# Performance work log

Hardware: AMD Instinct MI355X
Metric: run time of the kernel (lower is better)

Reference implementation:

```python
import jax, jax.numpy as jnp
import numpy as np

ALPHA = 0.2  # LeakyReLU negative slope


def _gat_layer(x, W, a):
    """One GraphAttentionLayer (concat=True -> elu output).
    x: (B,N,Din); W: (Din,F); a: (2F,1).
    Faithful to source: adj mask is computed then discarded (softmax over raw e),
    so adj does not enter the math. Uses the additive decomposition
    e_ij = leakyrelu(a1.h_i + a2.h_j) which is mathematically identical to the
    dense (N,N,2F) concat in the original.
    """
    h = x @ W                      # (B,N,F)
    F = W.shape[1]
    a1, a2 = a[:F, 0], a[F:, 0]    # (F,), (F,)
    f1 = h @ a1                    # (B,N)
    f2 = h @ a2                    # (B,N)
    e = jax.nn.leaky_relu(f1[:, :, None] + f2[:, None, :], negative_slope=ALPHA)  # (B,N,N)
    att = jax.nn.softmax(e, axis=-1)
    h_prime = jnp.einsum('bnm,bmf->bnf', att, h)
    return jax.nn.elu(h_prime)


def setup_inputs() -> dict:
    key = jax.random.key(0)
    ks = jax.random.split(key, 6)
    B, N, D, H, F = 8, 1024, 256, 8, 128
    x = jax.random.normal(ks[0], (B, N, D), jnp.float32)
    adj = (jax.random.uniform(ks[1], (N, N)) > 0.9).astype(jnp.float32)
    xavier = lambda fi, fo: 1.414 * (2.0 / (fi + fo)) ** 0.5
    W_heads = jax.random.normal(ks[2], (H, D, F), jnp.float32) * xavier(D, F)
    a_heads = jax.random.normal(ks[3], (H, 2 * F, 1), jnp.float32) * xavier(2 * F, 1)
    W_out = jax.random.normal(ks[4], (H * F, F), jnp.float32) * xavier(H * F, F)
    a_out = jax.random.normal(ks[5], (2 * F, 1), jnp.float32) * xavier(2 * F, 1)
    return {"x": x, "adj": adj, "W_heads": W_heads, "a_heads": a_heads,
            "W_out": W_out, "a_out": a_out}


def reference(x, adj, W_heads, a_heads, W_out, a_out):
    # GAT.forward (dropout omitted: eval mode identity). adj unused per source bug.
    heads = jax.vmap(lambda W, a: _gat_layer(x, W, a))(W_heads, a_heads)  # (H,B,N,F)
    B, N = x.shape[0], x.shape[1]
    xc = jnp.transpose(heads, (1, 2, 0, 3)).reshape(B, N, -1)  # concat heads: (B,N,H*F)
    # out_att has concat=True (applies elu), then GAT.forward applies elu again.
    return jax.nn.elu(_gat_layer(xc, W_out, a_out))
```

## Files before the change

kernel.cpp:

```cpp
#include <hip/hip_runtime.h>
#include <math.h>

#define ALPHA 0.2f
#define LOG2E 1.44269504089f

typedef __attribute__((ext_vector_type(8))) short bf16x8;
typedef __attribute__((ext_vector_type(4))) float f32x4;

__device__ __forceinline__ float elu1(float x)  { return x > 0.f ? x : (__expf(x) - 1.f); }

__device__ __forceinline__ unsigned short f2bf(float x) {
    unsigned u = __float_as_uint(x);
    return (unsigned short)((u + 0x7fffu + ((u >> 16) & 1u)) >> 16);
}
__device__ __forceinline__ unsigned pkbf16(float a, float b) {
    return (unsigned)f2bf(a) | ((unsigned)f2bf(b) << 16);
}
__device__ __forceinline__ float bflo(unsigned v) { return __uint_as_float(v << 16); }
__device__ __forceinline__ float bfhi(unsigned v) { return __uint_as_float(v & 0xffff0000u); }
__device__ __forceinline__ float bfs(unsigned short v) { return __uint_as_float((unsigned)v << 16); }
__device__ __forceinline__ unsigned pkbf_rhu(float a, float b) {
    unsigned ua = __float_as_uint(a) + 0x8000u;
    unsigned ub = __float_as_uint(b) + 0x8000u;
    return __builtin_amdgcn_perm(ub, ua, 0x07060302u);
}

__global__ __launch_bounds__(256) void cvt_w_all(
    const float* __restrict__ Wh, const float* __restrict__ Wo,
    unsigned short* __restrict__ WhT, unsigned short* __restrict__ WoT)
{
    const int z = blockIdx.z;
    const int K = (z < 8) ? 256 : 1024;
    if (blockIdx.x * 64 >= K) return;
    const float* in = (z < 8) ? (Wh + (size_t)z * K * 128) : Wo;
    unsigned short* out = (z < 8) ? (WhT + (size_t)z * 128 * K) : WoT;

    __shared__ float T[64][65];
    const int tid = threadIdx.x;
    const int k0 = blockIdx.x * 64, n0 = blockIdx.y * 64;

    const int kr = tid >> 4, nc = (tid & 15) * 4;
#pragma unroll
    for (int s = 0; s < 4; ++s) {
        float4 v = *(const float4*)(in + (size_t)(k0 + kr + s * 16) * 128 + n0 + nc);
        T[kr + s * 16][nc]     = v.x;
        T[kr + s * 16][nc + 1] = v.y;
        T[kr + s * 16][nc + 2] = v.z;
        T[kr + s * 16][nc + 3] = v.w;
    }
    __syncthreads();
    const int nr0 = tid >> 3, kc = (tid & 7) * 8;
#pragma unroll
    for (int s = 0; s < 2; ++s) {
        int nr = nr0 + s * 32;
        unsigned pk[4];
#pragma unroll
        for (int q = 0; q < 4; ++q)
            pk[q] = pkbf16(T[kc + 2 * q][nr], T[kc + 2 * q + 1][nr]);
        *(uint4*)(out + (size_t)(n0 + nr) * K + k0 + kc) = make_uint4(pk[0], pk[1], pk[2], pk[3]);
    }
}

template <int BM, int BN, int WM, int WN, int DOF, int AF32>
__global__ __launch_bounds__(256) void gemm_t(
    const void* __restrict__ Avp, const unsigned short* __restrict__ Bt,
    unsigned short* __restrict__ Ct, int K,
    const float* __restrict__ aV, float* __restrict__ f1g, float* __restrict__ f2g)
{
    const int RM = WM / 16, RN = WN / 16;
    const int NCA = BM * 8 / 256, NCB = BN * 8 / 256;
    __shared__ __align__(16) unsigned short SAB[(BM + BN) * 72];
    unsigned short (*As)[72] = (unsigned short(*)[72])SAB;
    unsigned short (*Bs)[72] = (unsigned short(*)[72])(SAB + BM * 72);
    unsigned short (*Cs)[BM + 8] = (unsigned short(*)[BM + 8])SAB;
    float* redf = (float*)(SAB + BN * (BM + 8));

    const int tid = threadIdx.x;
    const int w = tid >> 6, lane = tid & 63;
    const int n16 = lane & 15, quad = lane >> 4;
    const int WX = BM / WM;
    const int wm = (w % WX) * WM, wn = (w / WX) * WN;
    const int m0 = blockIdx.x * BM, n0 = blockIdx.y * BN;

    const float* Af = (const float*)Avp;
    const unsigned short* Ab = (const unsigned short*)Avp;
    const int ar = tid >> 2, akc = (tid & 3) * 16;

    f32x4 acc[RM][RN];
#pragma unroll
    for (int mm = 0; mm < RM; ++mm)
#pragma unroll
        for (int nn = 0; nn < RN; ++nn) acc[mm][nn] = (f32x4){0.f, 0.f, 0.f, 0.f};

    uint4 ra[NCA], rb[NCB];
    float4 raf[4];
    if (AF32) {
#pragma unroll
        for (int j = 0; j < 4; ++j)
            raf[j] = *(const float4*)(Af + (size_t)(m0 + ar) * K + akc + 4 * j);
    } else {
#pragma unroll
        for (int i = 0; i < NCA; ++i) {
            int c = tid * NCA + i, r = c >> 3, cc = (c & 7) * 8;
            ra[i] = *(const uint4*)(Ab + (size_t)(m0 + r) * K + cc);
        }
    }
#pragma unroll
    for (int i = 0; i < NCB; ++i) {
        int c = tid * NCB + i, r = c >> 3, cc = (c & 7) * 8;
        rb[i] = *(const uint4*)(Bt + (size_t)(n0 + r) * K + cc);
    }

    const int nk = K >> 6;
    for (int kt = 0; kt < nk; ++kt) {
        __syncthreads();
        if (AF32) {
            uint4 lo = make_uint4(pkbf16(raf[0].x, raf[0].y), pkbf16(raf[0].z, raf[0].w),
                                  pkbf16(raf[1].x, raf[1].y), pkbf16(raf[1].z, raf[1].w));
            uint4 hi = make_uint4(pkbf16(raf[2].x, raf[2].y), pkbf16(raf[2].z, raf[2].w),
                                  pkbf16(raf[3].x, raf[3].y), pkbf16(raf[3].z, raf[3].w));
            *(uint4*)&As[ar][akc]     = lo;
            *(uint4*)&As[ar][akc + 8] = hi;
        } else {
#pragma unroll
            for (int i = 0; i < NCA; ++i) {
                int c = tid * NCA + i, r = c >> 3, cc = (c & 7) * 8;
                *(uint4*)&As[r][cc] = ra[i];
            }
        }
#pragma unroll
        for (int i = 0; i < NCB; ++i) {
            int c = tid * NCB + i, r = c >> 3, cc = (c & 7) * 8;
            *(uint4*)&Bs[r][cc] = rb[i];
        }
        __syncthreads();
        if (kt + 1 < nk) {
            int k0 = (kt + 1) * 64;
            if (AF32) {
#pragma unroll
                for (int j = 0; j < 4; ++j)
                    raf[j] = *(const float4*)(Af + (size_t)(m0 + ar) * K + k0 + akc + 4 * j);
            } else {
#pragma unroll
                for (int i = 0; i < NCA; ++i) {
                    int c = tid * NCA + i, r = c >> 3, cc = (c & 7) * 8;
                    ra[i] = *(const uint4*)(Ab + (size_t)(m0 + r) * K + k0 + cc);
                }
            }
#pragma unroll
            for (int i = 0; i < NCB; ++i) {
                int c = tid * NCB + i, r = c >> 3, cc = (c & 7) * 8;
                rb[i] = *(const uint4*)(Bt + (size_t)(n0 + r) * K + k0 + cc);
            }
        }
#pragma unroll
        for (int ks = 0; ks < 2; ++ks) {
            bf16x8 am[RM], bn[RN];
#pragma unroll
            for (int mm = 0; mm < RM; ++mm)
                am[mm] = *(const bf16x8*)&As[wm + mm * 16 + n16][ks * 32 + quad * 8];
#pragma unroll
            for (int nn = 0; nn < RN; ++nn)
                bn[nn] = *(const bf16x8*)&Bs[wn + nn * 16 + n16][ks * 32 + quad * 8];
#pragma unroll
            for (int mm = 0; mm < RM; ++mm)
#pragma unroll
                for (int nn = 0; nn < RN; ++nn)
                    acc[mm][nn] = __builtin_amdgcn_mfma_f32_16x16x32_bf16(
                        am[mm], bn[nn], acc[mm][nn], 0, 0, 0);
        }
    }

    __syncthreads();

#pragma unroll
    for (int nn = 0; nn < RN; ++nn) {
        int n = wn + nn * 16 + n16;
#pragma unroll
        for (int mm = 0; mm < RM; ++mm) {
            int m = wm + mm * 16 + quad * 4;
            f32x4 a = acc[mm][nn];
            ushort4 o = make_ushort4(f2bf(a[0]), f2bf(a[1]), f2bf(a[2]), f2bf(a[3]));
            *(ushort4*)&Cs[n][m] = o;
        }
    }
    __syncthreads();

    const int CHUNKS = BM * 2 / 16;
    const int RPP = 256 / CHUNKS;
    const int row = tid / CHUNKS, ch = tid % CHUNKS;
#pragma unroll
    for (int s = 0; s < BN / RPP; ++s) {
        int n = row + s * RPP;
        *(uint4*)(Ct + (size_t)(n0 + n) * 8192 + m0 + ch * 8) =
            *(const uint4*)&Cs[n][ch * 8];
    }

    if (DOF) {
        const int G = 256 / BM;
        const int FP = 128 / G;
        const int mloc = tid % BM, fq = tid / BM;
        const float* az = aV + blockIdx.y * 256;
        float s1 = 0.f, s2 = 0.f;
#pragma unroll 8
        for (int k = 0; k < FP; ++k) {
            int f = fq * FP + k;
            float h = bfs(Cs[f][mloc]);
            s1 += h * az[f];
            s2 += h * az[128 + f];
        }
        *(float2*)&redf[(fq * BM + mloc) * 2] = make_float2(s1, s2);
        __syncthreads();
        if (tid < BM) {
            float a1 = 0.f, a2 = 0.f;
#pragma unroll
            for (int g = 0; g < G; ++g) {
                a1 += redf[(g * BM + tid) * 2];
                a2 += redf[(g * BM + tid) * 2 + 1];
            }
            f1g[(size_t)blockIdx.y * 8192 + m0 + tid] = a1;
            f2g[(size_t)blockIdx.y * 8192 + m0 + tid] = a2;
        }
    }
}

template <int NI, int OUTBF, int NT, int THREADS>
__global__ __launch_bounds__(THREADS) void attn4(
    const unsigned short* __restrict__ hT, const float* __restrict__ f1g,
    const float* __restrict__ f2g, float* __restrict__ outf,
    unsigned short* __restrict__ outb, int elu2)
{
    const int N = 1024, JT = 64, JP = 72;
    const int NW = THREADS / 64;
    const int ITILE = 16 * NI * NW;
    const int NTS = NT * 16 * 8 / THREADS;
    const int SR = THREADS / 8;
    __shared__ __align__(16) unsigned short hls[2][NT * 16][JP];
    __shared__ float ul[1024], vl[1024];
    __shared__ float wred[NW];

    const int tid = threadIdx.x;
    const int w = tid >> 6, lane = tid & 63;
    const int n16 = lane & 15, quad = lane >> 4;
    const int hy = OUTBF ? blockIdx.x : 0;
    const int bz = OUTBF ? blockIdx.z : blockIdx.x;
    const int fz = OUTBF ? 0 : blockIdx.z;
    const int ibx = blockIdx.y;
    const int hb = hy * 8 + bz;
    const int iw0 = ibx * ITILE + w * (16 * NI);

    if (THREADS == 256) {
        const int j4 = tid * 4;
        float4 fv = *(const float4*)(f2g + (size_t)hb * N + j4);
        fv.x *= LOG2E; fv.y *= LOG2E; fv.z *= LOG2E; fv.w *= LOG2E;
        *(float4*)&ul[j4] = fv;
        float m4 = fmaxf(fmaxf(fv.x, fv.y), fmaxf(fv.z, fv.w));
#pragma unroll
        for (int off = 32; off; off >>= 1) m4 = fmaxf(m4, __shfl_xor(m4, off));
        if (lane == 0) wred[w] = m4;
    } else {
        const int j2 = tid * 2;
        float2 fv = *(const float2*)(f2g + (size_t)hb * N + j2);
        fv.x *= LOG2E; fv.y *= LOG2E;
        *(float2*)&ul[j2] = fv;
        float m4 = fmaxf(fv.x, fv.y);
#pragma unroll
        for (int off = 32; off; off >>= 1) m4 = fmaxf(m4, __shfl_xor(m4, off));
        if (lane == 0) wred[w] = m4;
    }

    float f1L[NI];
#pragma unroll
    for (int ii = 0; ii < NI; ++ii)
        f1L[ii] = f1g[(size_t)hb * N + iw0 + ii * 16 + n16] * LOG2E;

    const unsigned short* gsrc = hT + (size_t)(hy * 128 + fz * (NT * 16)) * 8192 + bz * 1024;
    const int sf = tid >> 3, sj = (tid & 7) * 8;

    bf16x8 stg[NTS];
#pragma unroll
    for (int s = 0; s < NTS; ++s)
        stg[s] = *(const bf16x8*)(gsrc + (size_t)(sf + SR * s) * 8192 + sj);

    __syncthreads();
    float f2mL = wred[0];
#pragma unroll
    for (int k = 1; k < NW; ++k) f2mL = fmaxf(f2mL, wred[k]);

    if (THREADS == 256) {
        const int j4 = tid * 4;
        float4 raw = *(const float4*)&ul[j4];
        float4 uu, vv;
        float d0 = raw.x - f2mL, d1 = raw.y - f2mL, d2 = raw.z - f2mL, d3 = raw.w - f2mL;
        uu.x = __builtin_amdgcn_exp2f(d0); vv.x = __builtin_amdgcn_exp2f(ALPHA * d0);
        uu.y = __builtin_amdgcn_exp2f(d1); vv.y = __builtin_amdgcn_exp2f(ALPHA * d1);
        uu.z = __builtin_amdgcn_exp2f(d2); vv.z = __builtin_amdgcn_exp2f(ALPHA * d2);
        uu.w = __builtin_amdgcn_exp2f(d3); vv.w = __builtin_amdgcn_exp2f(ALPHA * d3);
        *(float4*)&ul[j4] = uu;
        *(float4*)&vl[j4] = vv;
    } else {
        const int j2 = tid * 2;
        float2 raw = *(const float2*)&ul[j2];
        float d0 = raw.x - f2mL, d1 = raw.y - f2mL;
        float2 uu, vv;
        uu.x = __builtin_amdgcn_exp2f(d0); vv.x = __builtin_amdgcn_exp2f(ALPHA * d0);
        uu.y = __builtin_amdgcn_exp2f(d1); vv.y = __builtin_amdgcn_exp2f(ALPHA * d1);
        *(float2*)&ul[j2] = uu;
        *(float2*)&vl[j2] = vv;
    }

    float ri[NI];
#pragma unroll
    for (int ii = 0; ii < NI; ++ii)
        ri[ii] = __builtin_amdgcn_exp2f((ALPHA - 1.f) * (f1L[ii] + f2mL));

    f32x4 acc[NI][NT], accl[NI];
#pragma unroll
    for (int ii = 0; ii < NI; ++ii) {
        accl[ii] = (f32x4){0.f, 0.f, 0.f, 0.f};
#pragma unroll
        for (int t = 0; t < NT; ++t) acc[ii][t] = (f32x4){0.f, 0.f, 0.f, 0.f};
    }
    bf16x8 ones;
    { union { bf16x8 v; unsigned u[4]; } o;
      o.u[0] = o.u[1] = o.u[2] = o.u[3] = 0x3F803F80u; ones = o.v; }

#pragma unroll
    for (int s = 0; s < NTS; ++s)
        *(bf16x8*)&hls[0][sf + SR * s][sj] = stg[s];
    __syncthreads();

    for (int jt = 0; jt < N / JT; ++jt) {
        const int cur = jt & 1;
        if (jt + 1 < N / JT) {
            int j0n = (jt + 1) * JT;
#pragma unroll
            for (int s = 0; s < NTS; ++s)
                stg[s] = *(const bf16x8*)(gsrc + (size_t)(sf + SR * s) * 8192 + j0n + sj);
        }
        const int j0 = jt * JT;
#pragma unroll
        for (int kk = 0; kk < 2; ++kk) {
            const int jb = j0 + kk * 32 + quad * 8;
            float4 u0 = *(const float4*)&ul[jb], u1 = *(const float4*)&ul[jb + 4];
            float4 v0 = *(const float4*)&vl[jb], v1 = *(const float4*)&vl[jb + 4];
            float uj[8] = {u0.x, u0.y, u0.z, u0.w, u1.x, u1.y, u1.z, u1.w};
            float vj[8] = {v0.x, v0.y, v0.z, v0.w, v1.x, v1.y, v1.z, v1.w};

            bf16x8 afr[NI];
#pragma unroll
            for (int ii = 0; ii < NI; ++ii) {
                union { bf16x8 v; unsigned u[4]; } cvt;
#pragma unroll
                for (int q = 0; q < 4; ++q) {
                    float p0 = fmaxf(uj[2 * q],     ri[ii] * vj[2 * q]);
                    float p1 = fmaxf(uj[2 * q + 1], ri[ii] * vj[2 * q + 1]);
                    cvt.u[q] = pkbf_rhu(p0, p1);
                }
                afr[ii] = cvt.v;
            }
#pragma unroll
            for (int t = 0; t < NT; ++t) {
                bf16x8 bfr = *(const bf16x8*)&hls[cur][t * 16 + n16][kk * 32 + quad * 8];
#pragma unroll
                for (int ii = 0; ii < NI; ++ii)
                    acc[ii][t] = __builtin_amdgcn_mfma_f32_16x16x32_bf16(
                        afr[ii], bfr, acc[ii][t], 0, 0, 0);
            }
#pragma unroll
            for (int ii = 0; ii < NI; ++ii)
                accl[ii] = __builtin_amdgcn_mfma_f32_16x16x32_bf16(
                    afr[ii], ones, accl[ii], 0, 0, 0);
        }
        if (jt + 1 < N / JT) {
#pragma unroll
            for (int s = 0; s < NTS; ++s)
                *(bf16x8*)&hls[1 - cur][sf + SR * s][sj] = stg[s];
        }
        __syncthreads();
    }

    if (OUTBF) {
        unsigned short (*Os)[140] = (unsigned short(*)[140])hls;
        const int WPP = 128 / (16 * NI);
#pragma unroll
        for (int pass = 0; pass < ITILE / 128; ++pass) {
            __syncthreads();
            if ((w / WPP) == pass) {
#pragma unroll
                for (int ii = 0; ii < NI; ++ii)
#pragma unroll
                    for (int r = 0; r < 4; ++r) {
                        float inv = 1.f / accl[ii][r];
                        int il = (w % WPP) * (16 * NI) + ii * 16 + quad * 4 + r;
#pragma unroll
                        for (int t = 0; t < NT; ++t)
                            Os[il][t * 16 + n16] = f2bf(elu1(acc[ii][t][r] * inv));
                    }
            }
            __syncthreads();
            {
                int orow = tid >> 2, q4 = tid & 3;
                size_t gb = (size_t)(bz * 1024 + ibx * ITILE + pass * 128 + orow) * 1024
                          + hy * 128 + q4 * 32;
                uint2 d[8];
#pragma unroll
                for (int s = 0; s < 8; ++s)
                    d[s] = *(const uint2*)&Os[orow][q4 * 32 + s * 4];
                *(uint4*)(outb + gb)      = make_uint4(d[0].x, d[0].y, d[1].x, d[1].y);
                *(uint4*)(outb + gb + 8)  = make_uint4(d[2].x, d[2].y, d[3].x, d[3].y);
                *(uint4*)(outb + gb + 16) = make_uint4(d[4].x, d[4].y, d[5].x, d[5].y);
                *(uint4*)(outb + gb + 24) = make_uint4(d[6].x, d[6].y, d[7].x, d[7].y);
            }
        }
    } else {
#pragma unroll
        for (int ii = 0; ii < NI; ++ii) {
#pragma unroll
            for (int r = 0; r < 4; ++r) {
                float inv = 1.f / accl[ii][r];
                int i = iw0 + ii * 16 + quad * 4 + r;
#pragma unroll
                for (int t = 0; t < NT; ++t) {
                    float tv = acc[ii][t][r] * inv;
                    tv = elu1(tv);
                    if (elu2) tv = elu1(tv);
                    outf[(size_t)(bz * 1024 + i) * 128 + fz * (NT * 16) + t * 16 + n16] = tv;
                }
            }
        }
    }
}

extern "C" void kernel_launch(void* const* d_in, const int* in_sizes, int n_in,
                              void* d_out, int out_size, void* d_ws, size_t ws_size,
                              hipStream_t stream)
{
    const float* x  = (const float*)d_in[0];
    const float* Wh = (const float*)d_in[2];
    const float* ah = (const float*)d_in[3];
    const float* Wo = (const float*)d_in[4];
    const float* ao = (const float*)d_in[5];
    float* out = (float*)d_out;

    unsigned short* WhT = (unsigned short*)d_ws;
    unsigned short* WoT = WhT + 262144;
    unsigned short* h1T = WoT + 131072;
    unsigned short* xcb = h1T + 8388608;
    unsigned short* h2T = xcb + 8388608;
    float* f1a  = (float*)(h2T + 1048576);
    float* f2a  = f1a + 65536;
    float* f1b  = f2a + 65536;
    float* f2b  = f1b + 8192;

    cvt_w_all<<<dim3(16, 2, 9), 256, 0, stream>>>(Wh, Wo, WhT, WoT);

    gemm_t<64, 128, 32, 64, 1, 1><<<dim3(128, 8), 256, 0, stream>>>(
        x, WhT, h1T, 256, ah, f1a, f2a);
    attn4<2, 1, 8, 512><<<dim3(8, 4, 8), 512, 0, stream>>>(h1T, f1a, f2a, nullptr, xcb, 0);

    gemm_t<32, 128, 16, 64, 1, 0><<<dim3(256, 1), 256, 0, stream>>>(
        xcb, WoT, h2T, 1024, ao, f1b, f2b);
    attn4<1, 0, 4, 256><<<dim3(8, 16, 2), 256, 0, stream>>>(h2T, f1b, f2b, out, nullptr, 1);
}
```

Baseline: 168.7 us.

## Specialize final attention kernel with full-tile LDS staging and enlarge first GEMM tile

The final attention layer moves to a dedicated kernel, attn5. It loads its whole 64-feature by 1024-node slice of h into LDS once, in place of double-buffering 64-column tiles, which removes the per-tile barriers and global-load staging. The first projection GEMM becomes a 128x128 tile with 512 threads, and attn4 drops the LDS-staged coalesced output path in favour of direct scattered bf16 stores. The ~130KB LDS footprint of attn5 limits residency to one block per CU. The direct 2-byte stores in attn4 may lower write efficiency.

```diff
diff --git a/kernel.cpp b/kernel.cpp
--- a/kernel.cpp
+++ b/kernel.cpp
@@ -16,8 +16,6 @@
 __device__ __forceinline__ unsigned pkbf16(float a, float b) {
     return (unsigned)f2bf(a) | ((unsigned)f2bf(b) << 16);
 }
-__device__ __forceinline__ float bflo(unsigned v) { return __uint_as_float(v << 16); }
-__device__ __forceinline__ float bfhi(unsigned v) { return __uint_as_float(v & 0xffff0000u); }
 __device__ __forceinline__ float bfs(unsigned short v) { return __uint_as_float((unsigned)v << 16); }
 __device__ __forceinline__ unsigned pkbf_rhu(float a, float b) {
     unsigned ua = __float_as_uint(a) + 0x8000u;
@@ -61,15 +59,18 @@
     }
 }
 
-template <int BM, int BN, int WM, int WN, int DOF, int AF32>
-__global__ __launch_bounds__(256) void gemm_t(
+template <int BM, int BN, int WM, int WN, int DOF, int AF32, int THREADS>
+__global__ __launch_bounds__(THREADS) void gemm_t(
     const void* __restrict__ Avp, const unsigned short* __restrict__ Bt,
     unsigned short* __restrict__ Ct, int K,
     const float* __restrict__ aV, float* __restrict__ f1g, float* __restrict__ f2g)
 {
     const int RM = WM / 16, RN = WN / 16;
-    const int NCA = BM * 8 / 256, NCB = BN * 8 / 256;
-    __shared__ __align__(16) unsigned short SAB[(BM + BN) * 72];
+    const int NCA = BM * 8 / THREADS, NCB = BN * 8 / THREADS;
+    constexpr int SAB_A = (BM + BN) * 72;
+    constexpr int SAB_B = BN * (BM + 8) + THREADS * 4;
+    constexpr int SAB_SH = SAB_A > SAB_B ? SAB_A : SAB_B;
+    __shared__ __align__(16) unsigned short SAB[SAB_SH];
     unsigned short (*As)[72] = (unsigned short(*)[72])SAB;
     unsigned short (*Bs)[72] = (unsigned short(*)[72])(SAB + BM * 72);
     unsigned short (*Cs)[BM + 8] = (unsigned short(*)[BM + 8])SAB;
@@ -92,7 +93,7 @@
 #pragma unroll
         for (int nn = 0; nn < RN; ++nn) acc[mm][nn] = (f32x4){0.f, 0.f, 0.f, 0.f};
 
-    uint4 ra[NCA], rb[NCB];
+    uint4 ra[NCA ? NCA : 1], rb[NCB];
     float4 raf[4];
     if (AF32) {
 #pragma unroll
@@ -187,7 +188,7 @@
     __syncthreads();
 
     const int CHUNKS = BM * 2 / 16;
-    const int RPP = 256 / CHUNKS;
+    const int RPP = THREADS / CHUNKS;
     const int row = tid / CHUNKS, ch = tid % CHUNKS;
 #pragma unroll
     for (int s = 0; s < BN / RPP; ++s) {
@@ -197,7 +198,7 @@
     }
 
     if (DOF) {
-        const int G = 256 / BM;
+        const int G = THREADS / BM;
         const int FP = 128 / G;
         const int mloc = tid % BM, fq = tid / BM;
         const float* az = aV + blockIdx.y * 256;
@@ -224,11 +225,10 @@
     }
 }
 
-template <int NI, int OUTBF, int NT, int THREADS>
+template <int NI, int NT, int THREADS>
 __global__ __launch_bounds__(THREADS) void attn4(
     const unsigned short* __restrict__ hT, const float* __restrict__ f1g,
-    const float* __restrict__ f2g, float* __restrict__ outf,
-    unsigned short* __restrict__ outb, int elu2)
+    const float* __restrict__ f2g, unsigned short* __restrict__ outb)
 {
     const int N = 1024, JT = 64, JP = 72;
     const int NW = THREADS / 64;
@@ -242,24 +242,14 @@
     const int tid = threadIdx.x;
     const int w = tid >> 6, lane = tid & 63;
     const int n16 = lane & 15, quad = lane >> 4;
-    const int hy = OUTBF ? blockIdx.x : 0;
-    const int bz = OUTBF ? blockIdx.z : blockIdx.x;
-    const int fz = OUTBF ? 0 : blockIdx.z;
+    const int hy = blockIdx.x;
+    const int bz = blockIdx.z;
     const int ibx = blockIdx.y;
     const int hb = hy * 8 + bz;
     const int iw0 = ibx * ITILE + w * (16 * NI);
 
-    if (THREADS == 256) {
-        const int j4 = tid * 4;
-        float4 fv = *(const float4*)(f2g + (size_t)hb * N + j4);
-        fv.x *= LOG2E; fv.y *= LOG2E; fv.z *= LOG2E; fv.w *= LOG2E;
-        *(float4*)&ul[j4] = fv;
-        float m4 = fmaxf(fmaxf(fv.x, fv.y), fmaxf(fv.z, fv.w));
-#pragma unroll
-        for (int off = 32; off; off >>= 1) m4 = fmaxf(m4, __shfl_xor(m4, off));
-        if (lane == 0) wred[w] = m4;
-    } else {
-        const int j2 = tid * 2;
+    {
+        const int j2 = tid * (1024 / THREADS);
         float2 fv = *(const float2*)(f2g + (size_t)hb * N + j2);
         fv.x *= LOG2E; fv.y *= LOG2E;
         *(float2*)&ul[j2] = fv;
@@ -274,7 +264,7 @@
     for (int ii = 0; ii < NI; ++ii)
         f1L[ii] = f1g[(size_t)hb * N + iw0 + ii * 16 + n16] * LOG2E;
 
-    const unsigned short* gsrc = hT + (size_t)(hy * 128 + fz * (NT * 16)) * 8192 + bz * 1024;
+    const unsigned short* gsrc = hT + (size_t)(hy * 128) * 8192 + bz * 1024;
     const int sf = tid >> 3, sj = (tid & 7) * 8;
 
     bf16x8 stg[NTS];
@@ -287,8 +277,148 @@
 #pragma unroll
     for (int k = 1; k < NW; ++k) f2mL = fmaxf(f2mL, wred[k]);
 
-    if (THREADS == 256) {
-        const int j4 = tid * 4;
+    {
+        const int j2 = tid * (1024 / THREADS);
+        float2 raw = *(const float2*)&ul[j2];
+        float d0 = raw.x - f2mL, d1 = raw.y - f2mL;
+        float2 uu, vv;
+        uu.x = __builtin_amdgcn_exp2f(d0); vv.x = __builtin_amdgcn_exp2f(ALPHA * d0);
+        uu.y = __builtin_amdgcn_exp2f(d1); vv.y = __builtin_amdgcn_exp2f(ALPHA * d1);
+        *(float2*)&ul[j2] = uu;
+        *(float2*)&vl[j2] = vv;
+    }
+
+    float ri[NI];
+#pragma unroll
+    for (int ii = 0; ii < NI; ++ii)
+        ri[ii] = __builtin_amdgcn_exp2f((ALPHA - 1.f) * (f1L[ii] + f2mL));
+
+    f32x4 acc[NI][NT], accl[NI];
+#pragma unroll
+    for (int ii = 0; ii < NI; ++ii) {
+        accl[ii] = (f32x4){0.f, 0.f, 0.f, 0.f};
+#pragma unroll
+        for (int t = 0; t < NT; ++t) acc[ii][t] = (f32x4){0.f, 0.f, 0.f, 0.f};
+    }
+    bf16x8 ones;
+    { union { bf16x8 v; unsigned u[4]; } o;
+      o.u[0] = o.u[1] = o.u[2] = o.u[3] = 0x3F803F80u; ones = o.v; }
+
+#pragma unroll
+    for (int s = 0; s < NTS; ++s)
+        *(bf16x8*)&hls[0][sf + SR * s][sj] = stg[s];
+    __syncthreads();
+
+    for (int jt = 0; jt < N / JT; ++jt) {
+        const int cur = jt & 1;
+        if (jt + 1 < N / JT) {
+            int j0n = (jt + 1) * JT;
+#pragma unroll
+            for (int s = 0; s < NTS; ++s)
+                stg[s] = *(const bf16x8*)(gsrc + (size_t)(sf + SR * s) * 8192 + j0n + sj);
+        }
+        const int j0 = jt * JT;
+#pragma unroll
+        for (int kk = 0; kk < 2; ++kk) {
+            const int jb = j0 + kk * 32 + quad * 8;
+            float4 u0 = *(const float4*)&ul[jb], u1 = *(const float4*)&ul[jb + 4];
+            float4 v0 = *(const float4*)&vl[jb], v1 = *(const float4*)&vl[jb + 4];
+            float uj[8] = {u0.x, u0.y, u0.z, u0.w, u1.x, u1.y, u1.z, u1.w};
+            float vj[8] = {v0.x, v0.y, v0.z, v0.w, v1.x, v1.y, v1.z, v1.w};
+
+            bf16x8 afr[NI];
+#pragma unroll
+            for (int ii = 0; ii < NI; ++ii) {
+                union { bf16x8 v; unsigned u[4]; } cvt;
+#pragma unroll
+                for (int q = 0; q < 4; ++q) {
+                    float p0 = fmaxf(uj[2 * q],     ri[ii] * vj[2 * q]);
+                    float p1 = fmaxf(uj[2 * q + 1], ri[ii] * vj[2 * q + 1]);
+                    cvt.u[q] = pkbf_rhu(p0, p1);
+                }
+                afr[ii] = cvt.v;
+            }
+#pragma unroll
+            for (int t = 0; t < NT; ++t) {
+                bf16x8 bfr = *(const bf16x8*)&hls[cur][t * 16 + n16][kk * 32 + quad * 8];
+#pragma unroll
+                for (int ii = 0; ii < NI; ++ii)
+                    acc[ii][t] = __builtin_amdgcn_mfma_f32_16x16x32_bf16(
+                        afr[ii], bfr, acc[ii][t], 0, 0, 0);
+            }
+#pragma unroll
+            for (int ii = 0; ii < NI; ++ii)
+                accl[ii] = __builtin_amdgcn_mfma_f32_16x16x32_bf16(
+                    afr[ii], ones, accl[ii], 0, 0, 0);
+        }
+        if (jt + 1 < N / JT) {
+#pragma unroll
+            for (int s = 0; s < NTS; ++s)
+                *(bf16x8*)&hls[1 - cur][sf + SR * s][sj] = stg[s];
+        }
+        __syncthreads();
+    }
+
+#pragma unroll
+    for (int ii = 0; ii < NI; ++ii) {
+#pragma unroll
+        for (int r = 0; r < 4; ++r) {
+            float inv = 1.f / accl[ii][r];
+            int i = iw0 + ii * 16 + quad * 4 + r;
+#pragma unroll
+            for (int t = 0; t < NT; ++t) {
+                float tv = acc[ii][t][r] * inv;
+                tv = elu1(tv);
+                outb[(size_t)(bz * 1024 + i) * 1024 + hy * 128 + t * 16 + n16] = f2bf(tv);
+            }
+        }
+    }
+}
+
+__global__ __launch_bounds__(256) void attn5(
+    const unsigned short* __restrict__ hT, const float* __restrict__ f1g,
+    const float* __restrict__ f2g, float* __restrict__ outf)
+{
+    const int N = 1024;
+    __shared__ __align__(16) unsigned short hfull[64][1032];
+    __shared__ float ul[1024], vl[1024];
+    __shared__ float wred[4];
+
+    const int tid = threadIdx.x;
+    const int w = tid >> 6, lane = tid & 63;
+    const int n16 = lane & 15, quad = lane >> 4;
+    const int bz = blockIdx.x;
+    const int ibx = blockIdx.y;
+    const int fz = blockIdx.z;
+    const int iw0 = ibx * 64 + w * 16;
+
+    const int j4 = tid * 4;
+    {
+        float4 fv = *(const float4*)(f2g + (size_t)bz * N + j4);
+        fv.x *= LOG2E; fv.y *= LOG2E; fv.z *= LOG2E; fv.w *= LOG2E;
+        *(float4*)&ul[j4] = fv;
+        float m4 = fmaxf(fmaxf(fv.x, fv.y), fmaxf(fv.z, fv.w));
+#pragma unroll
+        for (int off = 32; off; off >>= 1) m4 = fmaxf(m4, __shfl_xor(m4, off));
+        if (lane == 0) wred[w] = m4;
+    }
+
+    float f1L = f1g[(size_t)bz * N + iw0 + n16] * LOG2E;
+
+    const unsigned short* gsrc = hT + (size_t)(fz * 64) * 8192 + bz * 1024;
+    const int sr = tid >> 3;
+    const int sc = (tid & 7) * 8;
+#pragma unroll
+    for (int s = 0; s < 2; ++s)
+#pragma unroll
+        for (int c = 0; c < 16; ++c)
+            *(bf16x8*)&hfull[sr + 32 * s][sc + c * 64] =
+                *(const bf16x8*)(gsrc + (size_t)(sr + 32 * s) * 8192 + sc + c * 64);
+
+    __syncthreads();
+    const float f2mL = fmaxf(fmaxf(wred[0], wred[1]), fmaxf(wred[2], wred[3]));
+
+    {
         float4 raw = *(const float4*)&ul[j4];
         float4 uu, vv;
         float d0 = raw.x - f2mL, d1 = raw.y - f2mL, d2 = raw.z - f2mL, d3 = raw.w - f2mL;
@@ -298,136 +428,52 @@
         uu.w = __builtin_amdgcn_exp2f(d3); vv.w = __builtin_amdgcn_exp2f(ALPHA * d3);
         *(float4*)&ul[j4] = uu;
         *(float4*)&vl[j4] = vv;
-    } else {
-        const int j2 = tid * 2;
-        float2 raw = *(const float2*)&ul[j2];
-        float d0 = raw.x - f2mL, d1 = raw.y - f2mL;
-        float2 uu, vv;
-        uu.x = __builtin_amdgcn_exp2f(d0); vv.x = __builtin_amdgcn_exp2f(ALPHA * d0);
-        uu.y = __builtin_amdgcn_exp2f(d1); vv.y = __builtin_amdgcn_exp2f(ALPHA * d1);
-        *(float2*)&ul[j2] = uu;
-        *(float2*)&vl[j2] = vv;
-    }
-
-    float ri[NI];
-#pragma unroll
-    for (int ii = 0; ii < NI; ++ii)
-        ri[ii] = __builtin_amdgcn_exp2f((ALPHA - 1.f) * (f1L[ii] + f2mL));
-
-    f32x4 acc[NI][NT], accl[NI];
-#pragma unroll
-    for (int ii = 0; ii < NI; ++ii) {
-        accl[ii] = (f32x4){0.f, 0.f, 0.f, 0.f};
-#pragma unroll
-        for (int t = 0; t < NT; ++t) acc[ii][t] = (f32x4){0.f, 0.f, 0.f, 0.f};
-    }
+    }
+    const float ri = __builtin_amdgcn_exp2f((ALPHA - 1.f) * (f1L + f2mL));
+
+    f32x4 acc[4], accl = (f32x4){0.f, 0.f, 0.f, 0.f};
+#pragma unroll
+    for (int t = 0; t < 4; ++t) acc[t] = (f32x4){0.f, 0.f, 0.f, 0.f};
     bf16x8 ones;
     { union { bf16x8 v; unsigned u[4]; } o;
       o.u[0] = o.u[1] = o.u[2] = o.u[3] = 0x3F803F80u; ones = o.v; }
 
-#pragma unroll
-    for (int s = 0; s < NTS; ++s)
-        *(bf16x8*)&hls[0][sf + SR * s][sj] = stg[s];
-    __syncthreads();
-
-    for (int jt = 0; jt < N / JT; ++jt) {
-        const int cur = jt & 1;
-        if (jt + 1 < N / JT) {
-            int j0n = (jt + 1) * JT;
-#pragma unroll
-            for (int s = 0; s < NTS; ++s)
-                stg[s] = *(const bf16x8*)(gsrc + (size_t)(sf + SR * s) * 8192 + j0n + sj);
-        }
-        const int j0 = jt * JT;
+    __syncthreads();
+
+    for (int jt = 0; jt < 16; ++jt) {
 #pragma unroll
         for (int kk = 0; kk < 2; ++kk) {
-            const int jb = j0 + kk * 32 + quad * 8;
+            const int jb = jt * 64 + kk * 32 + quad * 8;
             float4 u0 = *(const float4*)&ul[jb], u1 = *(const float4*)&ul[jb + 4];
             float4 v0 = *(const float4*)&vl[jb], v1 = *(const float4*)&vl[jb + 4];
             float uj[8] = {u0.x, u0.y, u0.z, u0.w, u1.x, u1.y, u1.z, u1.w};
             float vj[8] = {v0.x, v0.y, v0.z, v0.w, v1.x, v1.y, v1.z, v1.w};
 
-            bf16x8 afr[NI];
-#pragma unroll
-            for (int ii = 0; ii < NI; ++ii) {
-                union { bf16x8 v; unsigned u[4]; } cvt;
-#pragma unroll
-                for (int q = 0; q < 4; ++q) {
-                    float p0 = fmaxf(uj[2 * q],     ri[ii] * vj[2 * q]);
-                    float p1 = fmaxf(uj[2 * q + 1], ri[ii] * vj[2 * q + 1]);
-                    cvt.u[q] = pkbf_rhu(p0, p1);
-                }
-                afr[ii] = cvt.v;
-            }
-#pragma unroll
-            for (int t = 0; t < NT; ++t) {
-                bf16x8 bfr = *(const bf16x8*)&hls[cur][t * 16 + n16][kk * 32 + quad * 8];
-#pragma unroll
-                for (int ii = 0; ii < NI; ++ii)
-                    acc[ii][t] = __builtin_amdgcn_mfma_f32_16x16x32_bf16(
-                        afr[ii], bfr, acc[ii][t], 0, 0, 0);
-            }
-#pragma unroll
-            for (int ii = 0; ii < NI; ++ii)
-                accl[ii] = __builtin_amdgcn_mfma_f32_16x16x32_bf16(
-                    afr[ii], ones, accl[ii], 0, 0, 0);
-        }
-        if (jt + 1 < N / JT) {
-#pragma unroll
-            for (int s = 0; s < NTS; ++s)
-                *(bf16x8*)&hls[1 - cur][sf + SR * s][sj] = stg[s];
-        }
-        __syncthreads();
-    }
-
-    if (OUTBF) {
-        unsigned short (*Os)[140] = (unsigned short(*)[140])hls;
-        const int WPP = 128 / (16 * NI);
-#pragma unroll
-        for (int pass = 0; pass < ITILE / 128; ++pass) {
-            __syncthreads();
-            if ((w / WPP) == pass) {
-#pragma unroll
-                for (int ii = 0; ii < NI; ++ii)
-#pragma unroll
-                    for (int r = 0; r < 4; ++r) {
-                        float inv = 1.f / accl[ii][r];
-                        int il = (w % WPP) * (16 * NI) + ii * 16 + quad * 4 + r;
-#pragma unroll
-                        for (int t = 0; t < NT; ++t)
-                            Os[il][t * 16 + n16] = f2bf(elu1(acc[ii][t][r] * inv));
-                    }
-            }
-            __syncthreads();
-            {
-                int orow = tid >> 2, q4 = tid & 3;
-                size_t gb = (size_t)(bz * 1024 + ibx * ITILE + pass * 128 + orow) * 1024
-                          + hy * 128 + q4 * 32;
-                uint2 d[8];
-#pragma unroll
-                for (int s = 0; s < 8; ++s)
-                    d[s] = *(const uint2*)&Os[orow][q4 * 32 + s * 4];
-                *(uint4*)(outb + gb)      = make_uint4(d[0].x, d[0].y, d[1].x, d[1].y);
-                *(uint4*)(outb + gb + 8)  = make_uint4(d[2].x, d[2].y, d[3].x, d[3].y);
-                *(uint4*)(outb + gb + 16) = make_uint4(d[4].x, d[4].y, d[5].x, d[5].y);
-                *(uint4*)(outb + gb + 24) = make_uint4(d[6].x, d[6].y, d[7].x, d[7].y);
-            }
-        }
-    } else {
-#pragma unroll
-        for (int ii = 0; ii < NI; ++ii) {
-#pragma unroll
-            for (int r = 0; r < 4; ++r) {
-                float inv = 1.f / accl[ii][r];
-                int i = iw0 + ii * 16 + quad * 4 + r;
-#pragma unroll
-                for (int t = 0; t < NT; ++t) {
-                    float tv = acc[ii][t][r] * inv;
-                    tv = elu1(tv);
-                    if (elu2) tv = elu1(tv);
-                    outf[(size_t)(bz * 1024 + i) * 128 + fz * (NT * 16) + t * 16 + n16] = tv;
-                }
-            }
+            union { bf16x8 v; unsigned u[4]; } cvt;
+#pragma unroll
+            for (int q = 0; q < 4; ++q) {
+                float p0 = fmaxf(uj[2 * q],     ri * vj[2 * q]);
+                float p1 = fmaxf(uj[2 * q + 1], ri * vj[2 * q + 1]);
+                cvt.u[q] = pkbf_rhu(p0, p1);
+            }
+            bf16x8 afr = cvt.v;
+#pragma unroll
+            for (int t = 0; t < 4; ++t) {
+                bf16x8 bfr = *(const bf16x8*)&hfull[t * 16 + n16][jb];
+                acc[t] = __builtin_amdgcn_mfma_f32_16x16x32_bf16(afr, bfr, acc[t], 0, 0, 0);
+            }
+            accl = __builtin_amdgcn_mfma_f32_16x16x32_bf16(afr, ones, accl, 0, 0, 0);
+        }
+    }
+
+#pragma unroll
+    for (int r = 0; r < 4; ++r) {
+        float inv = 1.f / accl[r];
+        int i = iw0 + quad * 4 + r;
+#pragma unroll
+        for (int t = 0; t < 4; ++t) {
+            float tv = elu1(elu1(acc[t][r] * inv));
+            outf[(size_t)(bz * 1024 + i) * 128 + fz * 64 + t * 16 + n16] = tv;
         }
     }
 }
@@ -455,11 +501,11 @@
 
     cvt_w_all<<<dim3(16, 2, 9), 256, 0, stream>>>(Wh, Wo, WhT, WoT);
 
-    gemm_t<64, 128, 32, 64, 1, 1><<<dim3(128, 8), 256, 0, stream>>>(
+    gemm_t<128, 128, 32, 64, 1, 1, 512><<<dim3(64, 8), 512, 0, stream>>>(
         x, WhT, h1T, 256, ah, f1a, f2a);
-    attn4<2, 1, 8, 512><<<dim3(8, 4, 8), 512, 0, stream>>>(h1T, f1a, f2a, nullptr, xcb, 0);
-
-    gemm_t<32, 128, 16, 64, 1, 0><<<dim3(256, 1), 256, 0, stream>>>(
+    attn4<2, 8, 512><<<dim3(8, 4, 8), 512, 0, stream>>>(h1T, f1a, f2a, xcb);
+
+    gemm_t<32, 128, 16, 64, 1, 0, 256><<<dim3(256, 1), 256, 0, stream>>>(
         xcb, WoT, h2T, 1024, ao, f1b, f2b);
-    attn4<1, 0, 4, 256><<<dim3(8, 16, 2), 256, 0, stream>>>(h2T, f1b, f2b, out, nullptr, 1);
-}
+    attn5<<<dim3(8, 16, 2), 256, 0, stream>>>(h2T, f1b, f2b, out);
+}
```

Result: faster. 153.9 us (-8.8%).
